# Kernel optimization log

Hardware: AMD Instinct MI355X
Metric: run time of the kernel (lower is better)

Reference implementation:

```python
import jax, jax.numpy as jnp
import numpy as np

B, N, CIN, COUT, K, L, NNZ = 4, 4096, 128, 128, 10, 50, 65536


def _spmm(idx, vals, X):
    # COO spmm: out[r] += vals * X[c]; idx: [2, nnz], X: [N, F]
    rows, cols = idx[0], idx[1]
    return jax.ops.segment_sum(vals[:, None] * X[cols], rows, num_segments=N)

_bspmm = jax.vmap(_spmm, in_axes=(0, 0, 0))  # batched over leading dim


def _hgnn_layer(phi_idx, phi_val, inv_idx, inv_val, fea, W, d):
    # original: ((phi @ diag(d)) @ phi_inv) @ (fea @ W)
    # identical math, evaluated right-to-left to stay sparse-dense only
    filt = jnp.einsum('bnc,co->bno', fea, W)            # [B,N,COUT]
    y = _bspmm(inv_idx, inv_val, filt)                  # phi_inv @ X
    y = d[None, :, None] * y                            # diag(d) @ .
    return _bspmm(phi_idx, phi_val, y)                  # phi @ .


def setup_inputs() -> dict:
    key = jax.random.key(0)
    ks = jax.random.split(key, 20)

    def coo(ki, kv):
        idx = jax.random.randint(ki, (B, 2, NNZ), 0, N, dtype=jnp.int32)
        val = jax.random.normal(kv, (B, NNZ), jnp.float32) * 0.05
        return idx, val

    phi1_idx, phi1_val = coo(ks[0], ks[1])
    phi1_inv_idx, phi1_inv_val = coo(ks[2], ks[3])
    phi2_idx, phi2_val = coo(ks[4], ks[5])
    phi2_inv_idx, phi2_inv_val = coo(ks[6], ks[7])
    fea = jax.random.normal(ks[8], (B, N, CIN), jnp.float32)
    joblst = jax.random.randint(ks[9], (B, L), 0, N, dtype=jnp.int64)

    xavier = float(np.sqrt(6.0 / (CIN + COUT)))
    W1 = jax.random.uniform(ks[10], (CIN, COUT), jnp.float32, -xavier, xavier)
    W2 = jax.random.uniform(ks[11], (CIN, COUT), jnp.float32, -xavier, xavier)
    d1 = jax.random.uniform(ks[12], (N,), jnp.float32, 0.9, 1.1)
    d2 = jax.random.uniform(ks[13], (N,), jnp.float32, 0.9, 1.1)
    s = float(1.0 / np.sqrt(N))
    W_ih = jax.random.uniform(ks[14], (N, COUT), jnp.float32, -s, s)
    W_hh = jax.random.uniform(ks[15], (N, N), jnp.float32, -s, s)
    b_ih = jax.random.uniform(ks[16], (N,), jnp.float32, -s, s)
    b_hh = jnp.zeros((N,), jnp.float32)
    sd = float(1.0 / np.sqrt(COUT))
    dense_W = jax.random.uniform(ks[17], (K, COUT), jnp.float32, -sd, sd)
    dense_b = jnp.zeros((K,), jnp.float32)
    item_emb = jax.random.normal(ks[18], (N, COUT), jnp.float32) * 0.01

    return dict(phi1_idx=phi1_idx, phi1_val=phi1_val, phi1_inv_idx=phi1_inv_idx,
                phi1_inv_val=phi1_inv_val, phi2_idx=phi2_idx, phi2_val=phi2_val,
                phi2_inv_idx=phi2_inv_idx, phi2_inv_val=phi2_inv_val,
                fea=fea, joblst=joblst, W1=W1, d1=d1, W2=W2, d2=d2,
                W_ih=W_ih, W_hh=W_hh, b_ih=b_ih, b_hh=b_hh,
                dense_W=dense_W, dense_b=dense_b, item_emb=item_emb)


def reference(phi1_idx, phi1_val, phi1_inv_idx, phi1_inv_val,
              phi2_idx, phi2_val, phi2_inv_idx, phi2_inv_val,
              fea, joblst, W1, d1, W2, d2, W_ih, W_hh, b_ih, b_hh,
              dense_W, dense_b, item_emb):
    # two hypergraph conv layers, summed
    out1 = _hgnn_layer(phi1_idx, phi1_val, phi1_inv_idx, phi1_inv_val, fea, W1, d1)
    out2 = _hgnn_layer(phi2_idx, phi2_val, phi2_inv_idx, phi2_inv_val, fea, W2, d2)
    res = out1 + out2                                   # [B,N,COUT]

    # RNN over job history embeddings (all joblst entries valid -> no -1 filter)
    xs = jnp.swapaxes(item_emb[joblst], 0, 1)           # [L,B,COUT]
    h0 = jnp.zeros((fea.shape[0], N), fea.dtype)

    def step(h, x):
        h = jnp.tanh(x @ W_ih.T + h @ W_hh.T + b_ih + b_hh)
        return h, None

    Emb, _ = jax.lax.scan(step, h0, xs)                 # last hidden: [B,N]

    res2 = jax.nn.gelu(jnp.einsum('bno,ko->bnk', res, dense_W) + dense_b,
                       approximate=False)               # [B,N,K]
    # (res3 * Emb2).permute back == res2 * gelu(Emb) broadcast over K
    return jax.nn.sigmoid(res2 * jax.nn.gelu(Emb, approximate=False)[:, :, None])
```

## Files before the change

kernel.cpp:

```cpp
#include <hip/hip_runtime.h>
#include <cstdint>
#include <cstddef>

#define NN   4096
#define LLC  50

__device__ __forceinline__ float bf2f(unsigned short u) {
    return __uint_as_float(((unsigned)u) << 16);
}
__device__ __forceinline__ unsigned short f2bf(float x) {
    unsigned b = __float_as_uint(x);
    return (unsigned short)((b + 0x7fffu + ((b >> 16) & 1u)) >> 16);
}

#if __has_builtin(__builtin_amdgcn_sdot4)
#define SDOT4(a, b, c) __builtin_amdgcn_sdot4((int)(a), (int)(b), (c), false)
#else
__device__ __forceinline__ int sdot4_sw(unsigned a, unsigned b, int c) {
    c += (int)(signed char)(a) * (int)(signed char)(b);
    c += (int)(signed char)(a >> 8) * (int)(signed char)(b >> 8);
    c += (int)(signed char)(a >> 16) * (int)(signed char)(b >> 16);
    c += (int)(signed char)(a >> 24) * (int)(signed char)(b >> 24);
    return c;
}
#define SDOT4(a, b, c) sdot4_sw((a), (b), (c))
#endif

#define DPPADD(v, ctrl, rmask) \
    ((v) + __builtin_amdgcn_update_dpp(0, (v), (ctrl), (rmask), 0xf, true))
__device__ __forceinline__ int wred64(int v) {
    v = DPPADD(v, 0x111, 0xf);
    v = DPPADD(v, 0x112, 0xf);
    v = DPPADD(v, 0x114, 0xf);
    v = DPPADD(v, 0x118, 0xf);
    v = DPPADD(v, 0x142, 0xa);
    v = DPPADD(v, 0x143, 0xc);
    return v;
}

__global__ __launch_bounds__(256) void k_w8(const float* __restrict__ W,
                                            uint4* __restrict__ out) {
    unsigned T = blockIdx.x * 256 + threadIdx.x;
    unsigned row = T >> 8, rem = T & 255;
    unsigned k4 = rem >> 6, lane = rem & 63;
    unsigned k0 = lane * 16 + k4 * 4;
    const float* src = W + ((size_t)row * 1024 + k0) * 4;
    unsigned q[4];
#pragma unroll
    for (int i = 0; i < 4; ++i) {
        float4 w = *(const float4*)(src + i * 4);
        int q0 = (int)rintf(fminf(fmaxf(w.x * 8192.f, -127.f), 127.f));
        int q1 = (int)rintf(fminf(fmaxf(w.y * 8192.f, -127.f), 127.f));
        int q2 = (int)rintf(fminf(fmaxf(w.z * 8192.f, -127.f), 127.f));
        int q3 = (int)rintf(fminf(fmaxf(w.w * 8192.f, -127.f), 127.f));
        q[i] = (q0 & 0xff) | ((q1 & 0xff) << 8) | ((q2 & 0xff) << 16) | ((q3 & 0xff) << 24);
    }
    out[(size_t)row * 256 + k4 * 64 + lane] = make_uint4(q[0], q[1], q[2], q[3]);
}

__global__ __launch_bounds__(128) void k_filt(const float* __restrict__ fea,
                                              const float* __restrict__ W1,
                                              const float* __restrict__ W2,
                                              unsigned short* __restrict__ f1,
                                              unsigned short* __restrict__ f2) {
    __shared__ float sfea[16][128];
    int t = threadIdx.x;
    int rb = blockIdx.x * 16;
    for (int r = 0; r < 16; ++r) sfea[r][t] = fea[(size_t)(rb + r) * 128 + t];
    __syncthreads();
    float a1[16], a2[16];
#pragma unroll
    for (int r = 0; r < 16; ++r) { a1[r] = 0.f; a2[r] = 0.f; }
    for (int c = 0; c < 128; c += 4) {
        float w10 = W1[(c + 0) * 128 + t], w11 = W1[(c + 1) * 128 + t];
        float w12 = W1[(c + 2) * 128 + t], w13 = W1[(c + 3) * 128 + t];
        float w20 = W2[(c + 0) * 128 + t], w21 = W2[(c + 1) * 128 + t];
        float w22 = W2[(c + 2) * 128 + t], w23 = W2[(c + 3) * 128 + t];
#pragma unroll
        for (int r = 0; r < 16; ++r) {
            float4 f = *(const float4*)&sfea[r][c];
            a1[r] += f.x * w10 + f.y * w11 + f.z * w12 + f.w * w13;
            a2[r] += f.x * w20 + f.y * w21 + f.z * w22 + f.w * w23;
        }
    }
#pragma unroll
    for (int r = 0; r < 16; ++r) {
        f1[(size_t)(rb + r) * 128 + t] = f2bf(a1[r]);
        f2[(size_t)(rb + r) * 128 + t] = f2bf(a2[r]);
    }
}

__global__ __launch_bounds__(256) void k_hist(const int* __restrict__ i0, const int* __restrict__ i1,
                                              const int* __restrict__ i2, const int* __restrict__ i3,
                                              int* __restrict__ counts) {
    __shared__ int lc[4096];
    int t = threadIdx.x;
#pragma unroll
    for (int i = 0; i < 16; ++i) lc[t + i * 256] = 0;
    __syncthreads();
    unsigned blk = blockIdx.x;
    unsigned s = blk >> 4, ch = blk & 15;
    unsigned m = s >> 2, b = s & 3;
    const int* ip = (m == 0) ? i0 : (m == 1) ? i1 : (m == 2) ? i2 : i3;
    unsigned base = b * 131072u + ch * 4096u;
#pragma unroll
    for (int i = 0; i < 16; ++i) {
        int r = ip[base + t + i * 256];
        atomicAdd(&lc[r], 1);
    }
    __syncthreads();
    int* cs = counts + s * 4096;
#pragma unroll
    for (int i = 0; i < 16; ++i) {
        int v = lc[t + i * 256];
        if (v) atomicAdd(cs + t + i * 256, v);
    }
}

__global__ __launch_bounds__(256) void k_scan(const int* __restrict__ counts,
                                              int* __restrict__ rowptr,
                                              int* __restrict__ cursor) {
    int s = blockIdx.x, t = threadIdx.x;
    int loc[16];
    int base = t * 16;
    const int* cs = counts + s * 4096;
    int run = 0;
#pragma unroll
    for (int i = 0; i < 16; ++i) { loc[i] = run; run += cs[base + i]; }
    int total = run;
    int lane = t & 63, wv = t >> 6;
    int v = total;
#pragma unroll
    for (int d = 1; d < 64; d <<= 1) { int u = __shfl_up(v, d, 64); if (lane >= d) v += u; }
    __shared__ int wt[4];
    if (lane == 63) wt[wv] = v;
    __syncthreads();
    int pre = v - total;
    for (int i = 0; i < wv; ++i) pre += wt[i];
    int* rp = rowptr + s * 4097;
    int* cu = cursor + s * 4096;
#pragma unroll
    for (int i = 0; i < 16; ++i) { rp[base + i] = pre + loc[i]; cu[base + i] = pre + loc[i]; }
    if (t == 255) rp[4096] = pre + total;
}

__global__ __launch_bounds__(256) void k_scatter(const int* __restrict__ i0, const int* __restrict__ i1,
                                                 const int* __restrict__ i2, const int* __restrict__ i3,
                                                 const float* __restrict__ v0, const float* __restrict__ v1,
                                                 const float* __restrict__ v2, const float* __restrict__ v3,
                                                 const float* __restrict__ d1, const float* __restrict__ d2,
                                                 int* __restrict__ cursor,
                                                 unsigned* __restrict__ ep) {
    unsigned gid = blockIdx.x * 256 + threadIdx.x;
    unsigned s = gid >> 16, e = gid & 65535;
    unsigned m = s >> 2, b = s & 3;
    const int* ip = (m == 0) ? i0 : (m == 1) ? i1 : (m == 2) ? i2 : i3;
    const float* vp = (m == 0) ? v0 : (m == 1) ? v1 : (m == 2) ? v2 : v3;
    int r = ip[(size_t)b * 131072 + e];
    int c = ip[(size_t)b * 131072 + 65536 + e];
    float v = vp[(size_t)b * 65536 + e];
    if (m == 1) v *= d1[c];
    if (m == 3) v *= d2[c];
    int pos = atomicAdd(cursor + s * 4096 + r, 1);
    ep[(size_t)s * 65536 + pos] = ((unsigned)c << 16) | (unsigned)f2bf(v);
}

__global__ __launch_bounds__(128) void k_gather1(const int* __restrict__ rowptr,
                                                 const unsigned* __restrict__ ep,
                                                 const unsigned short* __restrict__ filt1,
                                                 const unsigned short* __restrict__ filt2,
                                                 unsigned short* __restrict__ y1,
                                                 unsigned short* __restrict__ y2) {
    unsigned blk = blockIdx.x;
    unsigned b = blk & 3, row = (blk >> 2) & 4095, mm = blk >> 14;
    int s = (mm ? 8 : 0) + (int)b;
    const unsigned short* X = mm ? filt2 : filt1;
    unsigned short* Y = mm ? y2 : y1;
    int f = threadIdx.x;
    const int* rp = rowptr + s * 4097;
    int e0 = rp[row], e1 = rp[row + 1];
    float acc = 0.f;
    for (int e = e0; e < e1; ++e) {
        unsigned pp = ep[(size_t)s * 65536 + e];
        float v = bf2f((unsigned short)(pp & 0xffffu));
        int c = (int)(pp >> 16);
        acc += v * bf2f(X[((size_t)b * 4096 + c) * 128 + f]);
    }
    Y[((size_t)b * 4096 + row) * 128 + f] = f2bf(acc);
}

__global__ __launch_bounds__(128) void k_gather2(const int* __restrict__ rowptr,
                                                 const unsigned* __restrict__ ep,
                                                 const unsigned short* __restrict__ y1,
                                                 const unsigned short* __restrict__ y2,
                                                 float* __restrict__ res) {
    unsigned blk = blockIdx.x;
    unsigned b = blk & 3, row = blk >> 2;
    int f = threadIdx.x;
    float acc = 0.f;
    {
        int s = 4 + (int)b;
        const int* rp = rowptr + s * 4097;
        int e0 = rp[row], e1 = rp[row + 1];
        for (int e = e0; e < e1; ++e) {
            unsigned pp = ep[(size_t)s * 65536 + e];
            float v = bf2f((unsigned short)(pp & 0xffffu));
            int c = (int)(pp >> 16);
            acc += v * bf2f(y1[((size_t)b * 4096 + c) * 128 + f]);
        }
    }
    {
        int s = 12 + (int)b;
        const int* rp = rowptr + s * 4097;
        int e0 = rp[row], e1 = rp[row + 1];
        for (int e = e0; e < e1; ++e) {
            unsigned pp = ep[(size_t)s * 65536 + e];
            float v = bf2f((unsigned short)(pp & 0xffffu));
            int c = (int)(pp >> 16);
            acc += v * bf2f(y2[((size_t)b * 4096 + c) * 128 + f]);
        }
    }
    res[((size_t)b * 4096 + row) * 128 + f] = acc;
}

__global__ __launch_bounds__(256) void k_xproj(const float* __restrict__ item_emb,
                                               const int* __restrict__ joblst,
                                               const float* __restrict__ W_ih,
                                               const float* __restrict__ b_ih,
                                               const float* __restrict__ b_hh,
                                               float* __restrict__ xp) {
    __shared__ float sx[8][128];
    int t = threadIdx.x;
    int n = blockIdx.x * 256 + t;
    int p0 = blockIdx.y * 8;
#pragma unroll
    for (int i = 0; i < 4; ++i) {
        int e2 = t + i * 256;
        int rr = e2 >> 7, c = e2 & 127;
        int p = p0 + rr;
        int b = p & 3, l = p >> 2;
        int j = joblst[b * LLC + l];
        sx[rr][c] = item_emb[(size_t)j * 128 + c];
    }
    __syncthreads();
    float acc[8];
#pragma unroll
    for (int r = 0; r < 8; ++r) acc[r] = 0.f;
    const float* wn = W_ih + (size_t)n * 128;
    for (int c = 0; c < 128; c += 4) {
        float4 w = *(const float4*)(wn + c);
#pragma unroll
        for (int r = 0; r < 8; ++r) {
            float4 xr = *(const float4*)&sx[r][c];
            acc[r] += xr.x * w.x + xr.y * w.y + xr.z * w.z + xr.w * w.w;
        }
    }
    float bias = b_ih[n] + b_hh[n];
#pragma unroll
    for (int r = 0; r < 8; ++r) xp[(size_t)(p0 + r) * NN + n] = acc[r] + bias;
}

__global__ __launch_bounds__(256) void k_rnn_all(const uint4* __restrict__ Wp,
                                                 const float* __restrict__ xp,
                                                 unsigned* __restrict__ hq,
                                                 float* __restrict__ hfin,
                                                 int* __restrict__ bar) {
    __shared__ unsigned hs[4096];
    __shared__ int red[4][16];
    __shared__ unsigned char hpk[4][4][4];
    int t = threadIdx.x;
    int lane = t & 63, wv = t >> 6;
    int blk = blockIdx.x;
    int row_base = ((blk & 7) * 32 + (blk >> 3)) * 16;
    int wrow = row_base + wv * 4;

    uint4 W[4][4];
#pragma unroll
    for (int r = 0; r < 4; ++r)
#pragma unroll
        for (int k4 = 0; k4 < 4; ++k4)
            W[r][k4] = Wp[(size_t)(wrow + r) * 256 + k4 * 64 + lane];

    const float SC = 1.f / (8192.f * 127.f);

    for (int l = 0; l < LLC; ++l) {
        if (l > 0) {
            const unsigned* src = hq + (size_t)((l - 1) & 1) * 4096;
            unsigned sval[16];
#pragma unroll
            for (int k = 0; k < 16; ++k)
                sval[k] = __hip_atomic_load(src + t + k * 256, __ATOMIC_RELAXED,
                                            __HIP_MEMORY_SCOPE_AGENT);
#pragma unroll
            for (int k = 0; k < 16; ++k) hs[t + k * 256] = sval[k];
            __syncthreads();

            uint4 H[4][4];
#pragma unroll
            for (int b = 0; b < 4; ++b)
#pragma unroll
                for (int k4 = 0; k4 < 4; ++k4)
                    H[b][k4] = ((const uint4*)hs)[k4 * 256 + b * 64 + lane];
            int acc[4][4];
#pragma unroll
            for (int r = 0; r < 4; ++r)
#pragma unroll
                for (int b = 0; b < 4; ++b) acc[r][b] = 0;
#pragma unroll
            for (int k4 = 0; k4 < 4; ++k4)
#pragma unroll
                for (int r = 0; r < 4; ++r)
#pragma unroll
                    for (int b = 0; b < 4; ++b) {
                        acc[r][b] = SDOT4(W[r][k4].x, H[b][k4].x, acc[r][b]);
                        acc[r][b] = SDOT4(W[r][k4].y, H[b][k4].y, acc[r][b]);
                        acc[r][b] = SDOT4(W[r][k4].z, H[b][k4].z, acc[r][b]);
                        acc[r][b] = SDOT4(W[r][k4].w, H[b][k4].w, acc[r][b]);
                    }
#pragma unroll
            for (int r = 0; r < 4; ++r)
#pragma unroll
                for (int b = 0; b < 4; ++b) acc[r][b] = wred64(acc[r][b]);
            if (lane == 63) {
#pragma unroll
                for (int b = 0; b < 4; ++b) {
                    int4 q = { acc[0][b], acc[1][b], acc[2][b], acc[3][b] };
                    *(int4*)&red[wv][b * 4] = q;
                }
            }
        }
        if (lane < 16) {
            int b = lane >> 2, rr = lane & 3;
            int row = wrow + rr;
            float a = (l > 0) ? (float)red[wv][lane] * SC : 0.f;
            float pre = a + xp[(size_t)(l * 4 + b) * NN + row];
            float hnew = tanhf(pre);
            if (l == LLC - 1) hfin[(size_t)b * NN + row] = hnew;
            int q = (int)rintf(hnew * 127.f);
            hpk[wv][b][rr] = (unsigned char)(q & 0xff);
        }
        if (l < LLC - 1) {
            if (lane < 4) {
                int b = lane;
                unsigned d = *(const unsigned*)&hpk[wv][b][0];
                int hk = (row_base >> 2) + wv;
                int phys = ((hk >> 2) & 3) * 1024 + b * 256 + (hk >> 4) * 4 + (hk & 3);
                __hip_atomic_store(hq + (size_t)(l & 1) * 4096 + phys, d,
                                   __ATOMIC_RELAXED, __HIP_MEMORY_SCOPE_AGENT);
            }
            __syncthreads();
            if (t == 0) {
                int g = blk & 7;
                int old = __hip_atomic_fetch_add(&bar[g * 32], 1, __ATOMIC_RELAXED,
                                                 __HIP_MEMORY_SCOPE_AGENT);
                if ((old & 31) == 31)
                    __hip_atomic_fetch_add(&bar[256], 1, __ATOMIC_RELAXED,
                                           __HIP_MEMORY_SCOPE_AGENT);
                int target = 8 * (l + 1);
                while (__hip_atomic_load(&bar[256], __ATOMIC_RELAXED,
                                         __HIP_MEMORY_SCOPE_AGENT) < target)
                    __builtin_amdgcn_s_sleep(2);
            }
            __syncthreads();
        }
    }
}

__global__ __launch_bounds__(256) void k_final(const float* __restrict__ res,
                                               const float* __restrict__ dW,
                                               const float* __restrict__ db,
                                               const float* __restrict__ hfin,
                                               float* __restrict__ out) {
    __shared__ float4 sres4[512];
    __shared__ float sdw[10 * 132];
    int t = threadIdx.x;
    int row0 = blockIdx.x * 16;
    {
        const float4* src = (const float4*)(res + (size_t)row0 * 128);
        sres4[t] = src[t];
        sres4[t + 256] = src[t + 256];
    }
    for (int i = t; i < 1280; i += 256) { int k = i >> 7, c = i & 127; sdw[k * 132 + c] = dW[i]; }
    __syncthreads();
    int r = t >> 4, k = t & 15;
    if (k < 10) {
        const float* rr = (const float*)sres4 + r * 128;
        const float* wk = sdw + k * 132;
        float acc = 0.f;
#pragma unroll
        for (int c = 0; c < 128; c += 4) {
            float4 a = *(const float4*)(rr + c);
            float4 w = *(const float4*)(wk + c);
            acc += a.x * w.x + a.y * w.y + a.z * w.z + a.w * w.w;
        }
        float pre = acc + db[k];
        int grow = row0 + r;
        int b = grow >> 12, n = grow & 4095;
        float e = hfin[(size_t)b * NN + n];
        float g1 = 0.5f * pre * (1.f + erff(pre * 0.70710678118f));
        float ge = 0.5f * e * (1.f + erff(e * 0.70710678118f));
        out[(size_t)grow * 10 + k] = 1.f / (1.f + __expf(-g1 * ge));
    }
}

extern "C" void kernel_launch(void* const* d_in, const int* in_sizes, int n_in,
                              void* d_out, int out_size, void* d_ws, size_t ws_size,
                              hipStream_t stream) {
    const int*   phi1_idx = (const int*)d_in[0];
    const float* phi1_val = (const float*)d_in[1];
    const int*   inv1_idx = (const int*)d_in[2];
    const float* inv1_val = (const float*)d_in[3];
    const int*   phi2_idx = (const int*)d_in[4];
    const float* phi2_val = (const float*)d_in[5];
    const int*   inv2_idx = (const int*)d_in[6];
    const float* inv2_val = (const float*)d_in[7];
    const float* fea      = (const float*)d_in[8];
    const int*   joblst   = (const int*)d_in[9];
    const float* W1       = (const float*)d_in[10];
    const float* d1       = (const float*)d_in[11];
    const float* W2       = (const float*)d_in[12];
    const float* d2       = (const float*)d_in[13];
    const float* W_ih     = (const float*)d_in[14];
    const float* W_hh     = (const float*)d_in[15];
    const float* b_ih     = (const float*)d_in[16];
    const float* b_hh     = (const float*)d_in[17];
    const float* dense_W  = (const float*)d_in[18];
    const float* dense_b  = (const float*)d_in[19];
    const float* item_emb = (const float*)d_in[20];

    float* ws = (float*)d_ws;
    unsigned short* filt1 = (unsigned short*)ws;
    unsigned short* filt2 = (unsigned short*)(ws + 1048576);
    unsigned short* y1    = (unsigned short*)(ws + 2097152);
    unsigned short* y2    = (unsigned short*)(ws + 3145728);
    float* res  = ws + 4194304;
    float* xp   = ws + 6291456;
    float* hfin = ws + 7110656;
    unsigned* hq  = (unsigned*)(ws + 7127040);
    uint4* w8p = (uint4*)(ws + 7135232);
    int*   counts = (int*)(ws + 11329536);
    int*   rowptr = (int*)(ws + 11395072);
    int*   cursor = (int*)(ws + 11460624);
    unsigned* ep  = (unsigned*)(ws + 11526160);
    int*   bar    = (int*)(ws + 12574736);

    hipMemsetAsync(counts, 0, 16 * 4096 * sizeof(int), stream);
    hipMemsetAsync(bar, 0, 2048, stream);

    k_w8<<<4096, 256, 0, stream>>>(W_hh, w8p);
    k_filt<<<1024, 128, 0, stream>>>(fea, W1, W2, filt1, filt2);
    k_xproj<<<dim3(16, 25), 256, 0, stream>>>(item_emb, joblst, W_ih, b_ih, b_hh, xp);

    k_hist<<<256, 256, 0, stream>>>(inv1_idx, phi1_idx, inv2_idx, phi2_idx, counts);
    k_scan<<<16, 256, 0, stream>>>(counts, rowptr, cursor);
    k_scatter<<<4096, 256, 0, stream>>>(inv1_idx, phi1_idx, inv2_idx, phi2_idx,
                                        inv1_val, phi1_val, inv2_val, phi2_val,
                                        d1, d2, cursor, ep);

    k_gather1<<<32768, 128, 0, stream>>>(rowptr, ep, filt1, filt2, y1, y2);
    k_gather2<<<16384, 128, 0, stream>>>(rowptr, ep, y1, y2, res);

    k_rnn_all<<<256, 256, 0, stream>>>(w8p, xp, hq, hfin, bar);

    k_final<<<1024, 256, 0, stream>>>(res, dense_W, dense_b, hfin, (float*)d_out);
}
```

Baseline: 545.0 us.

## Fuse sparse gathers into RNN megakernel so SpMM overlaps the recurrent scan

Merges the two SpMM gather kernels and the persistent RNN kernel into one launch. Blocks 0-255 run the latency-bound RNN while blocks 256-511 do both SpMM stages, with an agent-scope barrier between stages and wider bf16x2 loads per lane. W_hh int8 quantisation moves into the RNN blocks' prologue, and s_setprio raises the RNN's priority during its dot products. The aim is to hide the SpMM and quantisation work behind the serial RNN, at the cost of shared CUs and the risk that the gather blocks slow the RNN or that co-residency assumptions fail.

```diff
diff --git a/kernel.cpp b/kernel.cpp
--- a/kernel.cpp
+++ b/kernel.cpp
@@ -36,26 +36,6 @@
     v = DPPADD(v, 0x142, 0xa);
     v = DPPADD(v, 0x143, 0xc);
     return v;
-}
-
-__global__ __launch_bounds__(256) void k_w8(const float* __restrict__ W,
-                                            uint4* __restrict__ out) {
-    unsigned T = blockIdx.x * 256 + threadIdx.x;
-    unsigned row = T >> 8, rem = T & 255;
-    unsigned k4 = rem >> 6, lane = rem & 63;
-    unsigned k0 = lane * 16 + k4 * 4;
-    const float* src = W + ((size_t)row * 1024 + k0) * 4;
-    unsigned q[4];
-#pragma unroll
-    for (int i = 0; i < 4; ++i) {
-        float4 w = *(const float4*)(src + i * 4);
-        int q0 = (int)rintf(fminf(fmaxf(w.x * 8192.f, -127.f), 127.f));
-        int q1 = (int)rintf(fminf(fmaxf(w.y * 8192.f, -127.f), 127.f));
-        int q2 = (int)rintf(fminf(fmaxf(w.z * 8192.f, -127.f), 127.f));
-        int q3 = (int)rintf(fminf(fmaxf(w.w * 8192.f, -127.f), 127.f));
-        q[i] = (q0 & 0xff) | ((q1 & 0xff) << 8) | ((q2 & 0xff) << 16) | ((q3 & 0xff) << 24);
-    }
-    out[(size_t)row * 256 + k4 * 64 + lane] = make_uint4(q[0], q[1], q[2], q[3]);
 }
 
 __global__ __launch_bounds__(128) void k_filt(const float* __restrict__ fea,
@@ -165,64 +145,6 @@
     ep[(size_t)s * 65536 + pos] = ((unsigned)c << 16) | (unsigned)f2bf(v);
 }
 
-__global__ __launch_bounds__(128) void k_gather1(const int* __restrict__ rowptr,
-                                                 const unsigned* __restrict__ ep,
-                                                 const unsigned short* __restrict__ filt1,
-                                                 const unsigned short* __restrict__ filt2,
-                                                 unsigned short* __restrict__ y1,
-                                                 unsigned short* __restrict__ y2) {
-    unsigned blk = blockIdx.x;
-    unsigned b = blk & 3, row = (blk >> 2) & 4095, mm = blk >> 14;
-    int s = (mm ? 8 : 0) + (int)b;
-    const unsigned short* X = mm ? filt2 : filt1;
-    unsigned short* Y = mm ? y2 : y1;
-    int f = threadIdx.x;
-    const int* rp = rowptr + s * 4097;
-    int e0 = rp[row], e1 = rp[row + 1];
-    float acc = 0.f;
-    for (int e = e0; e < e1; ++e) {
-        unsigned pp = ep[(size_t)s * 65536 + e];
-        float v = bf2f((unsigned short)(pp & 0xffffu));
-        int c = (int)(pp >> 16);
-        acc += v * bf2f(X[((size_t)b * 4096 + c) * 128 + f]);
-    }
-    Y[((size_t)b * 4096 + row) * 128 + f] = f2bf(acc);
-}
-
-__global__ __launch_bounds__(128) void k_gather2(const int* __restrict__ rowptr,
-                                                 const unsigned* __restrict__ ep,
-                                                 const unsigned short* __restrict__ y1,
-                                                 const unsigned short* __restrict__ y2,
-                                                 float* __restrict__ res) {
-    unsigned blk = blockIdx.x;
-    unsigned b = blk & 3, row = blk >> 2;
-    int f = threadIdx.x;
-    float acc = 0.f;
-    {
-        int s = 4 + (int)b;
-        const int* rp = rowptr + s * 4097;
-        int e0 = rp[row], e1 = rp[row + 1];
-        for (int e = e0; e < e1; ++e) {
-            unsigned pp = ep[(size_t)s * 65536 + e];
-            float v = bf2f((unsigned short)(pp & 0xffffu));
-            int c = (int)(pp >> 16);
-            acc += v * bf2f(y1[((size_t)b * 4096 + c) * 128 + f]);
-        }
-    }
-    {
-        int s = 12 + (int)b;
-        const int* rp = rowptr + s * 4097;
-        int e0 = rp[row], e1 = rp[row + 1];
-        for (int e = e0; e < e1; ++e) {
-            unsigned pp = ep[(size_t)s * 65536 + e];
-            float v = bf2f((unsigned short)(pp & 0xffffu));
-            int c = (int)(pp >> 16);
-            acc += v * bf2f(y2[((size_t)b * 4096 + c) * 128 + f]);
-        }
-    }
-    res[((size_t)b * 4096 + row) * 128 + f] = acc;
-}
-
 __global__ __launch_bounds__(256) void k_xproj(const float* __restrict__ item_emb,
                                                const int* __restrict__ joblst,
                                                const float* __restrict__ W_ih,
@@ -260,26 +182,131 @@
     for (int r = 0; r < 8; ++r) xp[(size_t)(p0 + r) * NN + n] = acc[r] + bias;
 }
 
-__global__ __launch_bounds__(256) void k_rnn_all(const uint4* __restrict__ Wp,
-                                                 const float* __restrict__ xp,
-                                                 unsigned* __restrict__ hq,
-                                                 float* __restrict__ hfin,
-                                                 int* __restrict__ bar) {
+template <bool AG>
+__device__ __forceinline__ unsigned ldx(const unsigned* p) {
+    if (AG) return __hip_atomic_load(p, __ATOMIC_RELAXED, __HIP_MEMORY_SCOPE_AGENT);
+    return *p;
+}
+
+template <bool AG>
+__device__ __forceinline__ void row_acc(const unsigned* __restrict__ eps, int e0, int e1,
+                                        const unsigned* __restrict__ Xd, unsigned bbase,
+                                        unsigned lane, float& a0, float& a1) {
+    int e = e0;
+    for (; e + 4 <= e1; e += 4) {
+        unsigned p0 = eps[e], p1 = eps[e + 1], p2 = eps[e + 2], p3 = eps[e + 3];
+        unsigned x0 = ldx<AG>(Xd + ((size_t)(bbase + (p0 >> 16)) << 6) + lane);
+        unsigned x1 = ldx<AG>(Xd + ((size_t)(bbase + (p1 >> 16)) << 6) + lane);
+        unsigned x2 = ldx<AG>(Xd + ((size_t)(bbase + (p2 >> 16)) << 6) + lane);
+        unsigned x3 = ldx<AG>(Xd + ((size_t)(bbase + (p3 >> 16)) << 6) + lane);
+        float v0 = bf2f((unsigned short)p0), v1 = bf2f((unsigned short)p1);
+        float v2 = bf2f((unsigned short)p2), v3 = bf2f((unsigned short)p3);
+        a0 += v0 * bf2f((unsigned short)x0); a1 += v0 * bf2f((unsigned short)(x0 >> 16));
+        a0 += v1 * bf2f((unsigned short)x1); a1 += v1 * bf2f((unsigned short)(x1 >> 16));
+        a0 += v2 * bf2f((unsigned short)x2); a1 += v2 * bf2f((unsigned short)(x2 >> 16));
+        a0 += v3 * bf2f((unsigned short)x3); a1 += v3 * bf2f((unsigned short)(x3 >> 16));
+    }
+    for (; e < e1; ++e) {
+        unsigned pp = eps[e];
+        unsigned xw = ldx<AG>(Xd + ((size_t)(bbase + (pp >> 16)) << 6) + lane);
+        float v = bf2f((unsigned short)pp);
+        a0 += v * bf2f((unsigned short)xw);
+        a1 += v * bf2f((unsigned short)(xw >> 16));
+    }
+}
+
+__global__ __launch_bounds__(256, 2) void k_mega(
+        const float* __restrict__ W_hh,
+        const float* __restrict__ xp,
+        unsigned* __restrict__ hq,
+        float* __restrict__ hfin,
+        int* __restrict__ bar,
+        const int* __restrict__ rowptr,
+        const unsigned* __restrict__ ep,
+        const unsigned short* __restrict__ filt1,
+        const unsigned short* __restrict__ filt2,
+        unsigned short* __restrict__ y1,
+        unsigned short* __restrict__ y2,
+        float* __restrict__ res) {
     __shared__ unsigned hs[4096];
     __shared__ int red[4][16];
     __shared__ unsigned char hpk[4][4][4];
     int t = threadIdx.x;
     int lane = t & 63, wv = t >> 6;
     int blk = blockIdx.x;
+
+    if (blk >= 256) {
+        int wid = (blk - 256) * 4 + wv;
+        {
+            unsigned mm = wid >> 9, b = (wid >> 7) & 3, rb = (wid & 127) * 32;
+            int s = (mm ? 8 : 0) + (int)b;
+            const unsigned* Xd = (const unsigned*)(mm ? filt2 : filt1);
+            unsigned* Yd = (unsigned*)(mm ? y2 : y1);
+            const int* rp = rowptr + s * 4097;
+            const unsigned* eps = ep + (size_t)s * 65536;
+            unsigned bbase = b * 4096;
+            for (int rr = 0; rr < 32; ++rr) {
+                int row = rb + rr;
+                float a0 = 0.f, a1 = 0.f;
+                row_acc<false>(eps, rp[row], rp[row + 1], Xd, bbase, lane, a0, a1);
+                unsigned pk = (unsigned)f2bf(a0) | ((unsigned)f2bf(a1) << 16);
+                __hip_atomic_store(Yd + ((size_t)(bbase + row) << 6) + lane, pk,
+                                   __ATOMIC_RELAXED, __HIP_MEMORY_SCOPE_AGENT);
+            }
+        }
+        __syncthreads();
+        if (t == 0) {
+            __hip_atomic_fetch_add(&bar[320], 1, __ATOMIC_RELAXED,
+                                   __HIP_MEMORY_SCOPE_AGENT);
+            while (__hip_atomic_load(&bar[320], __ATOMIC_RELAXED,
+                                     __HIP_MEMORY_SCOPE_AGENT) < 256)
+                __builtin_amdgcn_s_sleep(4);
+        }
+        __syncthreads();
+        {
+            unsigned b = wid >> 8, rb = (wid & 255) * 16;
+            unsigned bbase = b * 4096;
+            const int* rpA = rowptr + (4 + (int)b) * 4097;
+            const int* rpB = rowptr + (12 + (int)b) * 4097;
+            const unsigned* epA = ep + (size_t)(4 + b) * 65536;
+            const unsigned* epB = ep + (size_t)(12 + b) * 65536;
+            const unsigned* y1d = (const unsigned*)y1;
+            const unsigned* y2d = (const unsigned*)y2;
+            for (int rr = 0; rr < 16; ++rr) {
+                int row = rb + rr;
+                float a0 = 0.f, a1 = 0.f;
+                row_acc<true>(epA, rpA[row], rpA[row + 1], y1d, bbase, lane, a0, a1);
+                row_acc<true>(epB, rpB[row], rpB[row + 1], y2d, bbase, lane, a0, a1);
+                ((float2*)res)[((size_t)(bbase + row) << 6) + lane] = make_float2(a0, a1);
+            }
+        }
+        return;
+    }
+
     int row_base = ((blk & 7) * 32 + (blk >> 3)) * 16;
     int wrow = row_base + wv * 4;
 
     uint4 W[4][4];
-#pragma unroll
-    for (int r = 0; r < 4; ++r)
-#pragma unroll
-        for (int k4 = 0; k4 < 4; ++k4)
-            W[r][k4] = Wp[(size_t)(wrow + r) * 256 + k4 * 64 + lane];
+    {
+        const float* wsrc = W_hh + (size_t)wrow * 4096;
+#pragma unroll
+        for (int r = 0; r < 4; ++r)
+#pragma unroll
+            for (int k4 = 0; k4 < 4; ++k4) {
+                unsigned q[4];
+#pragma unroll
+                for (int i = 0; i < 4; ++i) {
+                    const float* p = wsrc + (size_t)r * 4096 + (lane * 16 + k4 * 4 + i) * 4;
+                    float4 w = *(const float4*)p;
+                    int q0 = (int)rintf(fminf(fmaxf(w.x * 8192.f, -127.f), 127.f));
+                    int q1 = (int)rintf(fminf(fmaxf(w.y * 8192.f, -127.f), 127.f));
+                    int q2 = (int)rintf(fminf(fmaxf(w.z * 8192.f, -127.f), 127.f));
+                    int q3 = (int)rintf(fminf(fmaxf(w.w * 8192.f, -127.f), 127.f));
+                    q[i] = (q0 & 0xff) | ((q1 & 0xff) << 8) | ((q2 & 0xff) << 16) | ((q3 & 0xff) << 24);
+                }
+                W[r][k4] = make_uint4(q[0], q[1], q[2], q[3]);
+            }
+    }
 
     const float SC = 1.f / (8192.f * 127.f);
 
@@ -295,6 +322,7 @@
             for (int k = 0; k < 16; ++k) hs[t + k * 256] = sval[k];
             __syncthreads();
 
+            __builtin_amdgcn_s_setprio(1);
             uint4 H[4][4];
 #pragma unroll
             for (int b = 0; b < 4; ++b)
@@ -328,6 +356,7 @@
                     *(int4*)&red[wv][b * 4] = q;
                 }
             }
+            __builtin_amdgcn_s_setprio(0);
         }
         if (lane < 16) {
             int b = lane >> 2, rr = lane & 3;
@@ -437,7 +466,6 @@
     float* xp   = ws + 6291456;
     float* hfin = ws + 7110656;
     unsigned* hq  = (unsigned*)(ws + 7127040);
-    uint4* w8p = (uint4*)(ws + 7135232);
     int*   counts = (int*)(ws + 11329536);
     int*   rowptr = (int*)(ws + 11395072);
     int*   cursor = (int*)(ws + 11460624);
@@ -447,7 +475,6 @@
     hipMemsetAsync(counts, 0, 16 * 4096 * sizeof(int), stream);
     hipMemsetAsync(bar, 0, 2048, stream);
 
-    k_w8<<<4096, 256, 0, stream>>>(W_hh, w8p);
     k_filt<<<1024, 128, 0, stream>>>(fea, W1, W2, filt1, filt2);
     k_xproj<<<dim3(16, 25), 256, 0, stream>>>(item_emb, joblst, W_ih, b_ih, b_hh, xp);
 
@@ -457,10 +484,8 @@
                                         inv1_val, phi1_val, inv2_val, phi2_val,
                                         d1, d2, cursor, ep);
 
-    k_gather1<<<32768, 128, 0, stream>>>(rowptr, ep, filt1, filt2, y1, y2);
-    k_gather2<<<16384, 128, 0, stream>>>(rowptr, ep, y1, y2, res);
-
-    k_rnn_all<<<256, 256, 0, stream>>>(w8p, xp, hq, hfin, bar);
+    k_mega<<<512, 256, 0, stream>>>(W_hh, xp, hq, hfin, bar,
+                                    rowptr, ep, filt1, filt2, y1, y2, res);
 
     k_final<<<1024, 256, 0, stream>>>(res, dense_W, dense_b, hfin, (float*)d_out);
 }
```

After: 529.4 us. -2.9%, faster.
